# Optimization experiments

Hardware: AMD Instinct MI355X
Metric: run time of the kernel (lower is better)

## Reference

```python
import jax, jax.numpy as jnp
import numpy as np

B, L, INP, HID, NCLS = 512, 256, 300, 256, 5  # trees, leaves/tree, embed dim, hidden, classes


def setup_inputs() -> dict:
    key = jax.random.key(0)
    ks = jax.random.split(key, 7)
    s_in = 1.0 / np.sqrt(INP).astype(np.float32)
    s_h = 1.0 / np.sqrt(HID).astype(np.float32)
    # W_leaf order: [inp_gate, out_gate, upd_gate]
    # W_nl order:  [inp_ln, inp_rn, fo_l_l, fo_l_r, fo_r_l, fo_r_r, out_ln, out_rn, upd_ln, upd_rn]
    return {
        "embeddings": jax.random.normal(ks[0], (B, L, INP), jnp.float32),
        "W_leaf": jax.random.uniform(ks[1], (3, INP, HID), jnp.float32, -s_in, s_in),
        "b_leaf": jax.random.uniform(ks[2], (3, HID), jnp.float32, -s_in, s_in),
        "W_nl": jax.random.uniform(ks[3], (10, HID, HID), jnp.float32, -s_h, s_h),
        "b_nl": jax.random.uniform(ks[4], (10, HID), jnp.float32, -s_h, s_h),
        "W_out": jax.random.uniform(ks[5], (HID, NCLS), jnp.float32, -s_h, s_h),
        "b_out": jax.random.uniform(ks[6], (NCLS,), jnp.float32, -s_h, s_h),
    }


def reference(embeddings, W_leaf, b_leaf, W_nl, b_nl, W_out, b_out):
    sig, tanh = jax.nn.sigmoid, jnp.tanh
    # ---- leaf nodes (depth 0), batched over all B*L leaves ----
    pre = jnp.einsum('bli,gih->blgh', embeddings, W_leaf) + b_leaf  # [B,L,3,H]
    i_g = sig(pre[:, :, 0])
    o_g = sig(pre[:, :, 1])
    u_g = tanh(pre[:, :, 2])
    c = i_g * u_g                      # [B,L,H]
    h = o_g * sig(c)                   # note: leaf uses sigmoid(cell), as in torch code
    logits = [jnp.einsum('bnh,hc->bnc', h, W_out) + b_out]
    # ---- internal nodes, level-synchronous ----
    Wl = W_nl[0::2]                    # [5,H,H] acting on left hidden
    Wr = W_nl[1::2]                    # [5,H,H] acting on right hidden
    bb = b_nl[0::2] + b_nl[1::2]       # [5,H]
    n = L
    while n > 1:
        lc, rc = c[:, 0::2], c[:, 1::2]
        lh, rh = h[:, 0::2], h[:, 1::2]
        pre = (jnp.einsum('bnh,ghk->bngk', lh, Wl)
               + jnp.einsum('bnh,ghk->bngk', rh, Wr) + bb)  # [B,n/2,5,H]
        inp_g = sig(pre[:, :, 0])
        fol_g = sig(pre[:, :, 1])
        for_g = sig(pre[:, :, 2])
        out_g = sig(pre[:, :, 3])
        upd_g = tanh(pre[:, :, 4])
        c = inp_g * upd_g + fol_g * lc + for_g * rc
        h = out_g * tanh(c)
        logits.append(jnp.einsum('bnh,hc->bnc', h, W_out) + b_out)
        n //= 2
    # per-node class scores for all 2L-1 nodes (leaves first, root last)
    return jnp.concatenate(logits, axis=1)  # [B, 2L-1, NCLS]
```

## Files before the change

### kernel.cpp

```cpp
#include <hip/hip_runtime.h>
#include <hip/hip_bf16.h>


#define HID 256

typedef __attribute__((ext_vector_type(8))) short short8;
typedef __attribute__((ext_vector_type(4))) float f32x4;
typedef __attribute__((ext_vector_type(4))) unsigned short ushort4v;

__device__ __forceinline__ float rcpf(float x) { return __builtin_amdgcn_rcpf(x); }
__device__ __forceinline__ float sigf(float x) { return rcpf(1.0f + __expf(-x)); }
__device__ __forceinline__ float tanhf_(float x) { return 2.0f * rcpf(1.0f + __expf(-2.0f * x)) - 1.0f; }
__device__ __forceinline__ unsigned short f2bf(float f) {
    __hip_bfloat16 b = __float2bfloat16(f);
    return *(unsigned short*)&b;
}
__device__ __forceinline__ void gload_lds16(const void* g, void* l) {
    __builtin_amdgcn_global_load_lds(
        (const __attribute__((address_space(1))) unsigned int*)g,
        (__attribute__((address_space(3))) unsigned int*)l, 16, 0, 0);
}

template <int NG, int K, bool LEAF>
__global__ __launch_bounds__(256, 2) void gemm_gates(
    const unsigned short* __restrict__ A,
    const unsigned short* __restrict__ BT,
    const float* __restrict__ bias,
    const float* __restrict__ cprev,
    float* __restrict__ cout,
    unsigned short* __restrict__ hout,
    const float* __restrict__ W_out,
    float* __restrict__ out,
    int log2n, int off)
{
    constexpr int BN = NG * 64;
    constexpr int NK = K / 64;
    constexpr int NBI = NG * 2;

    __shared__ char smem[(128 + BN) * 128];
    char* As = smem;
    char* Bs = smem + 128 * 128;

    const int t = threadIdx.x;
    const int lane = t & 63;
    const int w = t >> 6;
    const int wm = w >> 1, wn = w & 1;
    const int row0 = blockIdx.x * 128;
    const int cb = blockIdx.y;

    const int l3 = lane >> 3;
    const unsigned int swsrc = (unsigned int)(((lane & 7) ^ l3) * 16);
    unsigned int a_src[4];
    unsigned int b_src[NBI];
#pragma unroll
    for (int q = 0; q < 4; ++q) {
        int row = (w * 4 + q) * 8 + l3;
        a_src[q] = (unsigned int)(row0 + row) * (K * 2) + swsrc;
    }
#pragma unroll
    for (int q = 0; q < NBI; ++q) {
        int colp = (w * NBI + q) * 8 + l3;
        b_src[q] = (unsigned int)(cb * BN + colp) * (K * 2) + swsrc;
    }

    const int swz0 = ((lane >> 4) ^ (lane & 7)) * 16;
    const int swz1 = (((lane >> 4) + 4) ^ (lane & 7)) * 16;
    const int abase = (wm * 64 + (lane & 15)) * 128;
    const int bbase = (wn * 32 + (lane & 15)) * 128;

    f32x4 acc[4][NG * 2] = {};

    for (int kt = 0; kt < NK; ++kt) {
        const unsigned int k0b = kt * 128;
#pragma unroll
        for (int q = 0; q < 4; ++q)
            gload_lds16((const char*)A + (size_t)(a_src[q] + k0b),
                        As + (w * 4 + q) * 1024);
#pragma unroll
        for (int q = 0; q < NBI; ++q)
            gload_lds16((const char*)BT + (size_t)(b_src[q] + k0b),
                        Bs + (w * NBI + q) * 1024);
        __syncthreads();
#pragma unroll
        for (int ks = 0; ks < 2; ++ks) {
            const int sw = ks ? swz1 : swz0;
            short8 a[4];
#pragma unroll
            for (int mf = 0; mf < 4; ++mf)
                a[mf] = *(const short8*)(As + abase + mf * 2048 + sw);
#pragma unroll
            for (int g = 0; g < NG; ++g) {
                short8 b0 = *(const short8*)(Bs + bbase + g * 8192 + sw);
                short8 b1 = *(const short8*)(Bs + bbase + g * 8192 + 2048 + sw);
#pragma unroll
                for (int mf = 0; mf < 4; ++mf) {
                    acc[mf][g * 2 + 0] = __builtin_amdgcn_mfma_f32_16x16x32_bf16(
                        a[mf], b0, acc[mf][g * 2 + 0], 0, 0, 0);
                    acc[mf][g * 2 + 1] = __builtin_amdgcn_mfma_f32_16x16x32_bf16(
                        a[mf], b1, acc[mf][g * 2 + 1], 0, 0, 0);
                }
            }
        }
        __syncthreads();
    }

    float* hs = (float*)smem;
    float* Ws = (float*)(smem + 128 * 65 * 4);
    for (int i = t; i < 320; i += 256) Ws[i] = W_out[cb * 320 + i];

#pragma unroll
    for (int mf = 0; mf < 4; ++mf) {
#pragma unroll
        for (int j = 0; j < 4; ++j) {
            const int rl = wm * 64 + mf * 16 + ((lane >> 4) << 2) + j;
            const int r = row0 + rl;
#pragma unroll
            for (int fc = 0; fc < 2; ++fc) {
                const int cl = wn * 32 + fc * 16 + (lane & 15);
                const int c = cb * 64 + cl;
                float cv, hv;
                if constexpr (LEAF) {
                    float p0 = acc[mf][0 + fc][j] + bias[c];
                    float p1 = acc[mf][2 + fc][j] + bias[256 + c];
                    float p2 = acc[mf][4 + fc][j] + bias[512 + c];
                    cv = sigf(p0) * tanhf_(p2);
                    hv = sigf(p1) * sigf(cv);
                } else {
                    float p0 = acc[mf][0 + fc][j] + bias[c];
                    float p1 = acc[mf][2 + fc][j] + bias[256 + c];
                    float p2 = acc[mf][4 + fc][j] + bias[512 + c];
                    float p3 = acc[mf][6 + fc][j] + bias[768 + c];
                    float p4 = acc[mf][8 + fc][j] + bias[1024 + c];
                    float lc = cprev[(size_t)r * 512 + c];
                    float rc = cprev[(size_t)r * 512 + 256 + c];
                    cv = sigf(p0) * tanhf_(p4) + sigf(p1) * lc + sigf(p2) * rc;
                    hv = sigf(p3) * tanhf_(cv);
                }
                cout[(size_t)r * 256 + c] = cv;
                hout[(size_t)r * 256 + c] = f2bf(hv);
                hs[rl * 65 + cl] = hv;
            }
        }
    }
    __syncthreads();

    const int nmask = (1 << log2n) - 1;
    for (int idx = t; idx < 128 * 5; idx += 256) {
        int rl = idx / 5, cls = idx - rl * 5;
        float s = 0.f;
#pragma unroll
        for (int c2 = 0; c2 < 64; ++c2)
            s = fmaf(hs[rl * 65 + c2], Ws[c2 * 5 + cls], s);
        int rg = row0 + rl;
        int b = rg >> log2n, jj = rg & nmask;
        atomicAdd(out + ((size_t)b * 511 + off + jj) * 5 + cls, s);
    }
}

__global__ __launch_bounds__(256) void prep_weights(
    const float* __restrict__ W_leaf, const float* __restrict__ W_nl,
    const float* __restrict__ b_nl, const float* __restrict__ b_out,
    unsigned short* __restrict__ BleafT, unsigned short* __restrict__ BlevT,
    float* __restrict__ bb, float* __restrict__ out)
{
    const int T1 = 768 * 320, T2 = 1280 * 512, T3 = 5 * 256, T4 = 261632 * 5;
    for (int idx = blockIdx.x * 256 + threadIdx.x; idx < T1 + T2 + T3 + T4;
         idx += gridDim.x * 256) {
        if (idx < T1) {
            int colp = idx / 320, k = idx % 320;
            int cbv = colp / 192, rem = colp % 192;
            int g = rem >> 6, cl = rem & 63;
            int c = cbv * 64 + cl;
            float v = (k < 300) ? W_leaf[((size_t)g * 300 + k) * 256 + c] : 0.0f;
            BleafT[(size_t)colp * 320 + k] = f2bf(v);
        } else if (idx < T1 + T2) {
            int i2 = idx - T1;
            int colp = i2 / 512, k = i2 % 512;
            int cbv = colp / 320, rem = colp % 320;
            int g = rem >> 6, cl = rem & 63;
            int c = cbv * 64 + cl;
            float v = W_nl[((size_t)(2 * g + (k >= 256)) * 256 + (k & 255)) * 256 + c];
            BlevT[(size_t)colp * 512 + k] = f2bf(v);
        } else if (idx < T1 + T2 + T3) {
            int i3 = idx - T1 - T2;
            bb[i3] = b_nl[(size_t)(i3 >> 8) * 512 + (i3 & 255)] +
                     b_nl[(size_t)(i3 >> 8) * 512 + 256 + (i3 & 255)];
        } else {
            int i4 = idx - T1 - T2 - T3;
            out[i4] = b_out[i4 % 5];
        }
    }
}

__global__ __launch_bounds__(256) void emb_to_bf16(
    const float* __restrict__ emb, unsigned short* __restrict__ embB)
{
    const int total = 131072 * 80;
    for (int idx = blockIdx.x * 256 + threadIdx.x; idx < total;
         idx += gridDim.x * 256) {
        int r = idx / 80, q = idx % 80;
        ushort4v o;
        if (q < 75) {
            const float4 v = *(const float4*)(emb + (size_t)r * 300 + q * 4);
            o.x = f2bf(v.x); o.y = f2bf(v.y); o.z = f2bf(v.z); o.w = f2bf(v.w);
        } else {
            o.x = 0; o.y = 0; o.z = 0; o.w = 0;
        }
        *(ushort4v*)(embB + (size_t)r * 320 + q * 4) = o;
    }
}

extern "C" void kernel_launch(void* const* d_in, const int* in_sizes, int n_in,
                              void* d_out, int out_size, void* d_ws, size_t ws_size,
                              hipStream_t stream) {
    const float* emb    = (const float*)d_in[0];
    const float* W_leaf = (const float*)d_in[1];
    const float* b_leaf = (const float*)d_in[2];
    const float* W_nl   = (const float*)d_in[3];
    const float* b_nl   = (const float*)d_in[4];
    const float* W_out  = (const float*)d_in[5];
    const float* b_out  = (const float*)d_in[6];
    float* out = (float*)d_out;

    char* ws = (char*)d_ws;
    unsigned short* embB   = (unsigned short*)(ws);
    unsigned short* BleafT = (unsigned short*)(ws + 83886080);
    unsigned short* BlevT  = (unsigned short*)(ws + 84377600);
    float*          bb     = (float*)(ws + 85688320);
    float*          cA     = (float*)(ws + 85693440);
    unsigned short* hA     = (unsigned short*)(ws + 219911168);
    float*          cB     = (float*)(ws + 287020032);
    unsigned short* hB     = (unsigned short*)(ws + 354128896);

    prep_weights<<<2048, 256, 0, stream>>>(W_leaf, W_nl, b_nl, b_out,
                                           BleafT, BlevT, bb, out);
    emb_to_bf16<<<2048, 256, 0, stream>>>(emb, embB);

    gemm_gates<3, 320, true><<<dim3(1024, 4), 256, 0, stream>>>(
        embB, BleafT, b_leaf, nullptr, cA, hA, W_out, out, 8, 0);

    const unsigned short* hp = hA;
    const float* cp = cA;
    int off = 256;
    for (int lev = 1; lev <= 8; ++lev) {
        int log2n = 8 - lev;
        int n = 1 << log2n;
        int M = 512 * n;
        float* cd = (lev & 1) ? cB : cA;
        unsigned short* hd = (lev & 1) ? hB : hA;
        gemm_gates<5, 512, false><<<dim3(M / 128, 4), 256, 0, stream>>>(
            hp, BlevT, bb, cp, cd, hd, W_out, out, log2n, off);
        cp = cd;
        hp = hd;
        off += n;
    }
}
```

Measured before the change: 554.9 us.

## Double-buffer LDS K-loop and narrow level-GEMM column slices to 32

Adds double-buffered LDS staging in the gate GEMM so the next K-tile's global->LDS loads are issued before computing the current one, with a single barrier per iteration instead of two. Also parameterizes the per-gate column slice width (CS), using 32 columns for internal levels with twice as many column blocks, which gives small upper-tree levels more parallelism and lowers register pressure. The weight pre-transposition layout is changed to match. The cost is double the LDS footprint, which may hurt occupancy, and A tiles are re-read by more column blocks.

```diff
diff --git a/kernel.cpp b/kernel.cpp
--- a/kernel.cpp
+++ b/kernel.cpp
@@ -21,7 +21,7 @@
         (__attribute__((address_space(3))) unsigned int*)l, 16, 0, 0);
 }
 
-template <int NG, int K, bool LEAF>
+template <int NG, int CS, int K, bool LEAF>
 __global__ __launch_bounds__(256, 2) void gemm_gates(
     const unsigned short* __restrict__ A,
     const unsigned short* __restrict__ BT,
@@ -33,13 +33,13 @@
     float* __restrict__ out,
     int log2n, int off)
 {
-    constexpr int BN = NG * 64;
-    constexpr int NK = K / 64;
-    constexpr int NBI = NG * 2;
-
-    __shared__ char smem[(128 + BN) * 128];
-    char* As = smem;
-    char* Bs = smem + 128 * 128;
+    constexpr int BN  = NG * CS;
+    constexpr int NK  = K / 64;
+    constexpr int NF  = CS / 32;
+    constexpr int NBW = BN / 32;
+    constexpr int BUF = (128 + BN) * 128;
+
+    __shared__ char smem[2 * BUF];
 
     const int t = threadIdx.x;
     const int lane = t & 63;
@@ -51,62 +51,71 @@
     const int l3 = lane >> 3;
     const unsigned int swsrc = (unsigned int)(((lane & 7) ^ l3) * 16);
     unsigned int a_src[4];
-    unsigned int b_src[NBI];
-#pragma unroll
-    for (int q = 0; q < 4; ++q) {
-        int row = (w * 4 + q) * 8 + l3;
-        a_src[q] = (unsigned int)(row0 + row) * (K * 2) + swsrc;
-    }
-#pragma unroll
-    for (int q = 0; q < NBI; ++q) {
-        int colp = (w * NBI + q) * 8 + l3;
-        b_src[q] = (unsigned int)(cb * BN + colp) * (K * 2) + swsrc;
-    }
+    unsigned int b_src[NBW];
+#pragma unroll
+    for (int q = 0; q < 4; ++q)
+        a_src[q] = (unsigned int)(row0 + (w * 4 + q) * 8 + l3) * (K * 2) + swsrc;
+#pragma unroll
+    for (int q = 0; q < NBW; ++q)
+        b_src[q] = (unsigned int)(cb * BN + (w * NBW + q) * 8 + l3) * (K * 2) + swsrc;
 
     const int swz0 = ((lane >> 4) ^ (lane & 7)) * 16;
     const int swz1 = (((lane >> 4) + 4) ^ (lane & 7)) * 16;
-    const int abase = (wm * 64 + (lane & 15)) * 128;
-    const int bbase = (wn * 32 + (lane & 15)) * 128;
-
-    f32x4 acc[4][NG * 2] = {};
-
-    for (int kt = 0; kt < NK; ++kt) {
-        const unsigned int k0b = kt * 128;
+    const int aoff = (wm * 64 + (lane & 15)) * 128;
+    const int boff = (wn * (CS / 2) + (lane & 15)) * 128;
+
+    f32x4 acc[4][NG * NF] = {};
+
+    auto STAGE = [&](int buf, int kt) {
+        char* As = smem + buf * BUF;
+        char* Bs = As + 128 * 128;
+        const unsigned int k0b = (unsigned int)kt * 128;
 #pragma unroll
         for (int q = 0; q < 4; ++q)
             gload_lds16((const char*)A + (size_t)(a_src[q] + k0b),
                         As + (w * 4 + q) * 1024);
 #pragma unroll
-        for (int q = 0; q < NBI; ++q)
+        for (int q = 0; q < NBW; ++q)
             gload_lds16((const char*)BT + (size_t)(b_src[q] + k0b),
-                        Bs + (w * NBI + q) * 1024);
-        __syncthreads();
+                        Bs + (w * NBW + q) * 1024);
+    };
+
+    STAGE(0, 0);
+    asm volatile("s_waitcnt vmcnt(0)" ::: "memory");
+    __builtin_amdgcn_s_barrier();
+
+#pragma unroll
+    for (int kt = 0; kt < NK; ++kt) {
+        const int cur = kt & 1;
+        if (kt + 1 < NK) STAGE(cur ^ 1, kt + 1);
+        const char* As = smem + cur * BUF;
+        const char* Bs = As + 128 * 128;
 #pragma unroll
         for (int ks = 0; ks < 2; ++ks) {
             const int sw = ks ? swz1 : swz0;
             short8 a[4];
 #pragma unroll
             for (int mf = 0; mf < 4; ++mf)
-                a[mf] = *(const short8*)(As + abase + mf * 2048 + sw);
-#pragma unroll
-            for (int g = 0; g < NG; ++g) {
-                short8 b0 = *(const short8*)(Bs + bbase + g * 8192 + sw);
-                short8 b1 = *(const short8*)(Bs + bbase + g * 8192 + 2048 + sw);
-#pragma unroll
-                for (int mf = 0; mf < 4; ++mf) {
-                    acc[mf][g * 2 + 0] = __builtin_amdgcn_mfma_f32_16x16x32_bf16(
-                        a[mf], b0, acc[mf][g * 2 + 0], 0, 0, 0);
-                    acc[mf][g * 2 + 1] = __builtin_amdgcn_mfma_f32_16x16x32_bf16(
-                        a[mf], b1, acc[mf][g * 2 + 1], 0, 0, 0);
+                a[mf] = *(const short8*)(As + aoff + mf * 2048 + sw);
+#pragma unroll
+            for (int g = 0; g < NG; ++g)
+#pragma unroll
+                for (int fc = 0; fc < NF; ++fc) {
+                    short8 b = *(const short8*)(Bs + g * (CS * 128) + boff +
+                                                fc * 2048 + sw);
+#pragma unroll
+                    for (int mf = 0; mf < 4; ++mf)
+                        acc[mf][g * NF + fc] = __builtin_amdgcn_mfma_f32_16x16x32_bf16(
+                            a[mf], b, acc[mf][g * NF + fc], 0, 0, 0);
                 }
-            }
-        }
-        __syncthreads();
+        }
+        asm volatile("s_waitcnt vmcnt(0)" ::: "memory");
+        __builtin_amdgcn_s_barrier();
     }
 
     float* hs = (float*)smem;
-    float* Ws = (float*)(smem + 128 * 65 * 4);
-    for (int i = t; i < 320; i += 256) Ws[i] = W_out[cb * 320 + i];
+    float* Ws = (float*)(smem + 128 * (CS + 1) * 4);
+    for (int i = t; i < CS * 5; i += 256) Ws[i] = W_out[cb * CS * 5 + i];
 
 #pragma unroll
     for (int mf = 0; mf < 4; ++mf) {
@@ -115,22 +124,22 @@
             const int rl = wm * 64 + mf * 16 + ((lane >> 4) << 2) + j;
             const int r = row0 + rl;
 #pragma unroll
-            for (int fc = 0; fc < 2; ++fc) {
-                const int cl = wn * 32 + fc * 16 + (lane & 15);
-                const int c = cb * 64 + cl;
+            for (int fc = 0; fc < NF; ++fc) {
+                const int cl = wn * (CS / 2) + fc * 16 + (lane & 15);
+                const int c = cb * CS + cl;
                 float cv, hv;
                 if constexpr (LEAF) {
-                    float p0 = acc[mf][0 + fc][j] + bias[c];
-                    float p1 = acc[mf][2 + fc][j] + bias[256 + c];
-                    float p2 = acc[mf][4 + fc][j] + bias[512 + c];
+                    float p0 = acc[mf][0 * NF + fc][j] + bias[c];
+                    float p1 = acc[mf][1 * NF + fc][j] + bias[256 + c];
+                    float p2 = acc[mf][2 * NF + fc][j] + bias[512 + c];
                     cv = sigf(p0) * tanhf_(p2);
                     hv = sigf(p1) * sigf(cv);
                 } else {
-                    float p0 = acc[mf][0 + fc][j] + bias[c];
-                    float p1 = acc[mf][2 + fc][j] + bias[256 + c];
-                    float p2 = acc[mf][4 + fc][j] + bias[512 + c];
-                    float p3 = acc[mf][6 + fc][j] + bias[768 + c];
-                    float p4 = acc[mf][8 + fc][j] + bias[1024 + c];
+                    float p0 = acc[mf][0 * NF + fc][j] + bias[c];
+                    float p1 = acc[mf][1 * NF + fc][j] + bias[256 + c];
+                    float p2 = acc[mf][2 * NF + fc][j] + bias[512 + c];
+                    float p3 = acc[mf][3 * NF + fc][j] + bias[768 + c];
+                    float p4 = acc[mf][4 * NF + fc][j] + bias[1024 + c];
                     float lc = cprev[(size_t)r * 512 + c];
                     float rc = cprev[(size_t)r * 512 + 256 + c];
                     cv = sigf(p0) * tanhf_(p4) + sigf(p1) * lc + sigf(p2) * rc;
@@ -138,7 +147,7 @@
                 }
                 cout[(size_t)r * 256 + c] = cv;
                 hout[(size_t)r * 256 + c] = f2bf(hv);
-                hs[rl * 65 + cl] = hv;
+                hs[rl * (CS + 1) + cl] = hv;
             }
         }
     }
@@ -149,8 +158,8 @@
         int rl = idx / 5, cls = idx - rl * 5;
         float s = 0.f;
 #pragma unroll
-        for (int c2 = 0; c2 < 64; ++c2)
-            s = fmaf(hs[rl * 65 + c2], Ws[c2 * 5 + cls], s);
+        for (int c2 = 0; c2 < CS; ++c2)
+            s = fmaf(hs[rl * (CS + 1) + c2], Ws[c2 * 5 + cls], s);
         int rg = row0 + rl;
         int b = rg >> log2n, jj = rg & nmask;
         atomicAdd(out + ((size_t)b * 511 + off + jj) * 5 + cls, s);
@@ -176,9 +185,9 @@
         } else if (idx < T1 + T2) {
             int i2 = idx - T1;
             int colp = i2 / 512, k = i2 % 512;
-            int cbv = colp / 320, rem = colp % 320;
-            int g = rem >> 6, cl = rem & 63;
-            int c = cbv * 64 + cl;
+            int cb8 = colp / 160, rem = colp % 160;
+            int g = rem >> 5, cl = rem & 31;
+            int c = cb8 * 32 + cl;
             float v = W_nl[((size_t)(2 * g + (k >= 256)) * 256 + (k & 255)) * 256 + c];
             BlevT[(size_t)colp * 512 + k] = f2bf(v);
         } else if (idx < T1 + T2 + T3) {
@@ -236,7 +245,7 @@
                                            BleafT, BlevT, bb, out);
     emb_to_bf16<<<2048, 256, 0, stream>>>(emb, embB);
 
-    gemm_gates<3, 320, true><<<dim3(1024, 4), 256, 0, stream>>>(
+    gemm_gates<3, 64, 320, true><<<dim3(1024, 4), 256, 0, stream>>>(
         embB, BleafT, b_leaf, nullptr, cA, hA, W_out, out, 8, 0);
 
     const unsigned short* hp = hA;
@@ -248,7 +257,7 @@
         int M = 512 * n;
         float* cd = (lev & 1) ? cB : cA;
         unsigned short* hd = (lev & 1) ? hB : hA;
-        gemm_gates<5, 512, false><<<dim3(M / 128, 4), 256, 0, stream>>>(
+        gemm_gates<5, 32, 512, false><<<dim3(M / 128, 8), 256, 0, stream>>>(
             hp, BlevT, bb, cp, cd, hd, W_out, out, log2n, off);
         cp = cd;
         hp = hd;
```

Measured after the change: 502.3 us. 1.1x faster.
